# Performance work log

Hardware: AMD Instinct MI355X
Metric: run time of the kernel (lower is better)

## Reference

```python
import jax, jax.numpy as jnp
import numpy as np

N_NODES = 10000
N_EDGES = 5_000_000
BATCH = 2000


def setup_inputs() -> dict:
    key = jax.random.key(0)
    k1, k2, k3, k4 = jax.random.split(key, 4)
    n, E = N_NODES, N_EDGES
    # valid undirected pairs i < j
    i = jax.random.randint(k1, (E,), 0, n - 1)
    r = jax.random.randint(k2, (E,), 0, n)
    j = i + 1 + r % (n - 1 - i)
    edges = jnp.stack([i, j])  # [2, E], int
    edge_times = jax.random.uniform(k3, (E,), dtype=jnp.float32)
    edge_states = jax.random.randint(k4, (E,), 0, 2)
    return {
        "edges": edges,
        "edge_times": edge_times,
        "edge_states": edge_states,
        "nodes_num": n,
        "batch_size": BATCH,
    }


def _flat_idx(i, j, n):
    # undirected upper-triangular linearization of pair (i, j), i < j
    return i * n - i * (i + 1) // 2 + (j - i - 1)


def reference(edges, edge_times, edge_states, nodes_num, batch_size):
    n = nodes_num
    # -- multinomial(arange(n), batch_size, replacement=False) via Gumbel top-k --
    key = jax.random.key(19)
    w = jnp.arange(n, dtype=jnp.float32)
    logw = jnp.where(w > 0, jnp.log(jnp.maximum(w, 1.0)), -jnp.inf)
    scores = logw + jax.random.gumbel(key, (n,), dtype=jnp.float32)
    _, sel = jax.lax.top_k(scores, batch_size)
    batch_nodes = jnp.sort(sel)

    # -- all combinations (i < j since batch_nodes is sorted) --
    ii, jj = np.triu_indices(batch_size, k=1)  # static shapes
    batch_pairs = jnp.stack([batch_nodes[ii], batch_nodes[jj]])  # [2, P]
    batch_flat = _flat_idx(batch_pairs[0], batch_pairs[1], n)  # ascending

    # -- gather stored edges whose pair index is in the batch --
    edge_flat = _flat_idx(edges[0], edges[1], n)
    order = jnp.argsort(edge_flat)  # jax sort is stable -> matches coalesce order
    edges_sorted = edges[:, order]
    flat_sorted = edge_flat[order]
    times_sorted = edge_times[order]
    states_sorted = edge_states[order]

    pos = jnp.searchsorted(batch_flat, flat_sorted)
    pos = jnp.clip(pos, 0, batch_flat.shape[0] - 1)
    mask = batch_flat[pos] == flat_sorted  # [E] membership of each edge in batch

    batch_edge_times = jnp.where(mask, times_sorted, 0.0)
    batch_states = jnp.where(mask, states_sorted, 0)
    return (batch_nodes, batch_pairs, edges_sorted, batch_edge_times,
            batch_states, mask)
```

## Files before the change

kernel.cpp:

```cpp
#include <hip/hip_runtime.h>
#include <stdint.h>
#include <math.h>

#define N_NODES  10000
#define N_EDGES  5000000
#define BATCH    2000
#define N_PAIRS  1999000

#define OUT_BN      0
#define OUT_PAIRS0  2000
#define OUT_PAIRS1  2001000
#define OUT_ES0     4000000
#define OUT_ES1     9000000
#define OUT_T       14000000
#define OUT_S       19000000
#define OUT_M       24000000

#define WS_KEYS     0
#define WS_SEL      80000
#define WS_BN       120000
#define WS_CNT      128000
#define WS_FILL     168000
#define WS_OFF      208000
#define WS_SCRATCH  248064


#define RPB_LOG  7
#define NB1      79
#define CHUNK    2048
#define NBIN     192
#define NBITSW   313
#define RANK_BLKS 200

typedef unsigned long long u64;

__device__ __forceinline__ u64 score_key(int w, unsigned bits) {
  const float TINY = 1.17549435e-38f;
  float uf = __uint_as_float((bits >> 9) | 0x3f800000u) - 1.0f;
  float val = fmaxf(TINY, uf + TINY);
  float t1 = (float)log((double)val);
  float gmb = -(float)log((double)(-t1));
  float score = (w > 0) ? ((float)log((double)w) + gmb) : (-INFINITY);
  unsigned fb = __float_as_uint(score);
  unsigned s = (fb & 0x80000000u) ? ~fb : (fb | 0x80000000u);
  unsigned d = ~s;
  return ((u64)d << 32) | (unsigned)w;
}

__device__ __forceinline__ u64 make_key(int v) {
  unsigned ks[3] = {0u, 19u, 0u ^ 19u ^ 0x1BD11BDAu};
  unsigned x0 = 0u + ks[0];
  unsigned x1 = (unsigned)v + ks[1];
  const int R0[4] = {13, 15, 26, 6};
  const int R1[4] = {17, 29, 16, 24};
#pragma unroll
  for (int g = 0; g < 5; ++g) {
    const int* R = (g & 1) ? R1 : R0;
#pragma unroll
    for (int r = 0; r < 4; ++r) {
      x0 += x1;
      x1 = (x1 << R[r]) | (x1 >> (32 - R[r]));
      x1 ^= x0;
    }
    x0 += ks[(g + 1) % 3];
    x1 += ks[(g + 2) % 3] + (unsigned)(g + 1);
  }
  return score_key(v, x0 ^ x1);
}

__global__ void __launch_bounds__(256) k_rankhist(
    int* __restrict__ rankc, int* __restrict__ cnt,
    const int4* __restrict__ e_i4) {
  __shared__ __align__(16) int sh4[N_NODES];
  int tid = threadIdx.x;
  if ((int)blockIdx.x < RANK_BLKS) {
    u64* lk = (u64*)sh4;
    int vblk = blockIdx.x / 5, cblk = blockIdx.x % 5;
    int base = cblk * 2048;
    int lenc = min(2048, N_NODES - base);
    for (int t = tid; t < lenc; t += 256) lk[t] = make_key(base + t);
    __syncthreads();
    int v = vblk * 256 + tid;
    u64 kv = (v < N_NODES) ? make_key(v) : 0;
    int c = 0;
    for (int t = 0; t < lenc; ++t) c += (lk[t] < kv) ? 1 : 0;
    if (v < N_NODES && c) atomicAdd(&rankc[v], c);
  } else {
    int* h = sh4;
    for (int t = tid; t < N_NODES; t += 256) h[t] = 0;
    __syncthreads();
    int hb = blockIdx.x - RANK_BLKS;
    int stride = 256 * 256;
    for (int t = hb * 256 + tid; t < N_EDGES / 4; t += stride) {
      int4 r = e_i4[t];
      atomicAdd(&h[r.x], 1);
      atomicAdd(&h[r.y], 1);
      atomicAdd(&h[r.z], 1);
      atomicAdd(&h[r.w], 1);
    }
    __syncthreads();
    for (int t = tid; t < N_NODES; t += 256) {
      int c = h[t];
      if (c) atomicAdd(&cnt[t], c);
    }
  }
}

__global__ void k_scan_all(const int* rankc, int* sel, int* bn, float* outbn,
                           const int* cnt, int* off, int* fill, int* fill1,
                           unsigned* selbits) {
  __shared__ int wsum[16];
  __shared__ unsigned lb[320];
  const int PER = 10;
  int tid = threadIdx.x, lane = tid & 63, wid = tid >> 6;
  int base = tid * PER;
  int svv[PER];
  {
    int s = 0;
#pragma unroll
    for (int k = 0; k < PER; ++k) {
      int i = base + k;
      if (i < N_NODES) {
        int sv = (rankc[i] < BATCH) ? 1 : 0;
        sel[i] = sv;
        svv[k] = sv;
        s += sv;
      } else svv[k] = 0;
    }
    int inc = s;
#pragma unroll
    for (int d = 1; d < 64; d <<= 1) {
      int v = __shfl_up(inc, d, 64);
      if (lane >= d) inc += v;
    }
    if (lane == 63) wsum[wid] = inc;
    __syncthreads();
    int woff = 0;
    for (int w = 0; w < wid; ++w) woff += wsum[w];
    int run = woff + inc - s;
#pragma unroll
    for (int k = 0; k < PER; ++k) {
      int i = base + k;
      if (i < N_NODES && svv[k]) {
        bn[run] = i;
        outbn[run] = (float)i;
        ++run;
      }
    }
  }
  __syncthreads();
  {
    int cv[PER];
    int s = 0;
#pragma unroll
    for (int k = 0; k < PER; ++k) {
      int i = base + k;
      if (i < N_NODES) { cv[k] = cnt[i]; s += cv[k]; } else cv[k] = 0;
    }
    int inc = s;
#pragma unroll
    for (int d = 1; d < 64; d <<= 1) {
      int v = __shfl_up(inc, d, 64);
      if (lane >= d) inc += v;
    }
    if (lane == 63) wsum[wid] = inc;
    __syncthreads();
    int woff = 0;
    for (int w = 0; w < wid; ++w) woff += wsum[w];
    int run = woff + inc - s;
#pragma unroll
    for (int k = 0; k < PER; ++k) {
      int i = base + k;
      if (i < N_NODES) {
        off[i] = run;
        fill[i] = run;
        if ((i & ((1 << RPB_LOG) - 1)) == 0) fill1[i >> RPB_LOG] = run;
        run += cv[k];
      }
    }
    if (tid == 0) off[N_NODES] = N_EDGES;
  }
  __syncthreads();
  if (tid < 320) lb[tid] = 0;
  __syncthreads();
#pragma unroll
  for (int k = 0; k < PER; ++k) {
    int i = base + k;
    if (i < N_NODES && svv[k]) atomicOr(&lb[i >> 5], 1u << (i & 31));
  }
  __syncthreads();
  if (tid < NBITSW) selbits[tid] = lb[tid];
}

__global__ void __launch_bounds__(256) k_pairs_part1(
    const int* __restrict__ e_i, const int* __restrict__ e_j,
    const int* __restrict__ st, int* __restrict__ fill1,
    u64* __restrict__ stage, const int* __restrict__ bn,
    float* __restrict__ outp, int nblk1) {
  __shared__ u64 lkey[CHUNK];
  __shared__ int h[NB1], bstart[NB1], basec[NB1], cur[NB1];
  __shared__ int tcount_s;
  int tid = threadIdx.x;
  if ((int)blockIdx.x >= nblk1) {
    int p = ((int)blockIdx.x - nblk1) * 256 + tid;
    if (p >= N_PAIRS) return;
    float tf = 2.0f * BATCH - 1.0f;
    float disc = tf * tf - 8.0f * (float)p;
    int ii = (int)((tf - sqrtf(disc)) * 0.5f);
    if (ii < 0) ii = 0;
    if (ii > BATCH - 2) ii = BATCH - 2;
    while (ii > 0 &&
           (long long)ii * (BATCH - 1) - (long long)ii * (ii - 1) / 2 > p) --ii;
    while ((long long)(ii + 1) * (BATCH - 1) - (long long)(ii + 1) * ii / 2 <= p) ++ii;
    long long S = (long long)ii * (BATCH - 1) - (long long)ii * (ii - 1) / 2;
    int jj = ii + 1 + (int)(p - S);
    outp[p] = (float)bn[ii];
    outp[N_PAIRS + p] = (float)bn[jj];
    return;
  }
  int c0 = (int)blockIdx.x * CHUNK;
  int nloc = min(CHUNK, N_EDGES - c0);
  for (int t = tid; t < NB1; t += 256) h[t] = 0;
  __syncthreads();
  int iv[CHUNK / 256];
  const int4* e_i4 = (const int4*)(e_i + c0);
#pragma unroll
  for (int k = 0; k < CHUNK / 1024; ++k) {
    int q = tid + 256 * k;
    int ebase = 4 * q;
    if (ebase < nloc) {
      int4 r = e_i4[q];
      iv[4 * k + 0] = r.x; iv[4 * k + 1] = r.y;
      iv[4 * k + 2] = r.z; iv[4 * k + 3] = r.w;
      atomicAdd(&h[r.x >> RPB_LOG], 1);
      atomicAdd(&h[r.y >> RPB_LOG], 1);
      atomicAdd(&h[r.z >> RPB_LOG], 1);
      atomicAdd(&h[r.w >> RPB_LOG], 1);
    } else {
      iv[4 * k + 0] = iv[4 * k + 1] = iv[4 * k + 2] = iv[4 * k + 3] = -1;
    }
  }
  __syncthreads();
  if (tid < 64) {
    int a = h[tid];
    int b = (tid + 64 < NB1) ? h[tid + 64] : 0;
    int inc0 = a;
#pragma unroll
    for (int d = 1; d < 64; d <<= 1) {
      int v = __shfl_up(inc0, d, 64);
      if (tid >= d) inc0 += v;
    }
    int t0 = __shfl(inc0, 63, 64);
    int inc1 = b;
#pragma unroll
    for (int d = 1; d < 64; d <<= 1) {
      int v = __shfl_up(inc1, d, 64);
      if (tid >= d) inc1 += v;
    }
    int tot = t0 + __shfl(inc1, 63, 64);
    bstart[tid] = inc0 - a;
    if (tid + 64 < NB1) bstart[tid + 64] = t0 + inc1 - b;
    if (tid == 0) tcount_s = tot;
  }
  __syncthreads();
  for (int b = tid; b < NB1; b += 256) {
    basec[b] = h[b] ? atomicAdd(&fill1[b], h[b]) : 0;
    cur[b] = bstart[b];
  }
  __syncthreads();
  const int4* e_j4 = (const int4*)(e_j + c0);
  const int4* st4 = (const int4*)(st + c0);
#pragma unroll
  for (int k = 0; k < CHUNK / 1024; ++k) {
    int q = tid + 256 * k;
    int ebase = 4 * q;
    if (ebase < nloc) {
      int4 jj = e_j4[q];
      int4 ss = st4[q];
      int js[4] = {jj.x, jj.y, jj.z, jj.w};
      int s4[4] = {ss.x, ss.y, ss.z, ss.w};
#pragma unroll
      for (int c = 0; c < 4; ++c) {
        int i = iv[4 * k + c];
        unsigned e = (unsigned)(c0 + ebase + c);
        int b = i >> RPB_LOG;
        int pos = atomicAdd(&cur[b], 1);
        lkey[pos] = ((u64)(unsigned)i << 38) | ((u64)(unsigned)js[c] << 24) |
                    ((u64)e << 1) | (u64)(unsigned)s4[c];
      }
    }
  }
  __syncthreads();
  int tcount = tcount_s;
  for (int t = tid; t < tcount; t += 256) {
    u64 kv = lkey[t];
    int b = (int)(kv >> (38 + RPB_LOG));
    stage[basec[b] + (t - bstart[b])] = kv;
  }
}

__global__ void __launch_bounds__(256) k_part2(
    const u64* __restrict__ stage, int* __restrict__ fill,
    u64* __restrict__ sk) {
  __shared__ u64 lkey[CHUNK];
  __shared__ int h[256], bstart[256], baser[256], cur[256], wsum4[4];
  __shared__ int rowbase_s;
  int tid = threadIdx.x, lane = tid & 63, wid = tid >> 6;
  int c0 = (int)blockIdx.x * CHUNK;
  int nloc = min(CHUNK, N_EDGES - c0);
  h[tid] = 0;
  if (tid == 0)
    rowbase_s = ((int)(stage[c0] >> (38 + RPB_LOG))) << RPB_LOG;
  __syncthreads();
  int rowbase = rowbase_s;
  u64 kv[CHUNK / 256];
#pragma unroll
  for (int k = 0; k < CHUNK / 256; ++k) {
    int q = tid + 256 * k;
    if (q < nloc) {
      kv[k] = stage[c0 + q];
      atomicAdd(&h[(int)(kv[k] >> 38) - rowbase], 1);
    }
  }
  __syncthreads();
  int hv = h[tid];
  int inc = hv;
#pragma unroll
  for (int d = 1; d < 64; d <<= 1) {
    int v = __shfl_up(inc, d, 64);
    if (lane >= d) inc += v;
  }
  if (lane == 63) wsum4[wid] = inc;
  __syncthreads();
  int woff = 0;
  for (int w = 0; w < wid; ++w) woff += wsum4[w];
  int tcount = wsum4[0] + wsum4[1] + wsum4[2] + wsum4[3];
  int excl = woff + inc - hv;
  bstart[tid] = excl;
  cur[tid] = excl;
  baser[tid] = hv ? atomicAdd(&fill[rowbase + tid], hv) : 0;
  __syncthreads();
#pragma unroll
  for (int k = 0; k < CHUNK / 256; ++k) {
    int q = tid + 256 * k;
    if (q < nloc) {
      int lr = (int)(kv[k] >> 38) - rowbase;
      int pos = atomicAdd(&cur[lr], 1);
      lkey[pos] = kv[k];
    }
  }
  __syncthreads();
  for (int t = tid; t < tcount; t += 256) {
    u64 v = lkey[t];
    int lr = (int)(v >> 38) - rowbase;
    sk[baser[lr] + (t - bstart[lr])] = v;
  }
}

__global__ void __launch_bounds__(256) k_rowsort_key(
    const u64* __restrict__ sk, const int* __restrict__ off,
    const float* __restrict__ times, const unsigned* __restrict__ selbits,
    float* __restrict__ out) {
  __shared__ u64 buf[768];
  __shared__ int hist[NBIN], cur[NBIN];
  __shared__ unsigned bits[320];
  int tid = threadIdx.x;
  int row = blockIdx.x;
  int o0 = off[row], o1 = off[row + 1];
  int len = o1 - o0;
  if (len <= 0) return;
  if (len > 768) len = 768;
  int span = N_NODES - 1 - row;
  int s = 0;
  while ((span >> s) >= 160) ++s;
  int mi = (int)((selbits[row >> 5] >> (row & 31)) & 1u);
  for (int t = tid; t < NBIN; t += 256) hist[t] = 0;
  if (mi) {
    for (int t = tid; t < NBITSW; t += 256) bits[t] = selbits[t];
  }
  __syncthreads();
  u64 kv[3];
  int dv[3], rv[3];
  int jbase = row + 1;
#pragma unroll
  for (int k = 0; k < 3; ++k) {
    int t = tid + 256 * k;
    if (t < len) {
      u64 v = sk[o0 + t];
      kv[k] = v;
      int j = (int)((v >> 24) & 0x3FFFull);
      int d = (j - jbase) >> s;
      dv[k] = d;
      atomicAdd(&hist[d], 1);
    } else {
      dv[k] = -1;
    }
  }
  __syncthreads();
  if (tid < 64) {
    int b0 = tid * 3;
    int c0 = hist[b0], c1 = hist[b0 + 1], c2 = hist[b0 + 2];
    int sum = c0 + c1 + c2;
    int inc = sum;
#pragma unroll
    for (int d = 1; d < 64; d <<= 1) {
      int v = __shfl_up(inc, d, 64);
      if (tid >= d) inc += v;
    }
    int excl = inc - sum;
    hist[b0] = excl;
    hist[b0 + 1] = excl + c0;
    hist[b0 + 2] = excl + c0 + c1;
    cur[b0] = excl;
    cur[b0 + 1] = excl + c0;
    cur[b0 + 2] = excl + c0 + c1;
  }
  __syncthreads();
#pragma unroll
  for (int k = 0; k < 3; ++k) {
    if (dv[k] >= 0) {
      int pos = atomicAdd(&cur[dv[k]], 1);
      buf[pos] = kv[k];
    }
  }
  __syncthreads();
#pragma unroll
  for (int k = 0; k < 3; ++k) {
    if (dv[k] >= 0) {
      u64 me = kv[k];
      int s0 = hist[dv[k]];
      int s1 = cur[dv[k]];
      int r = 0;
      for (int q = s0; q < s1; ++q) r += (buf[q] < me) ? 1 : 0;
      rv[k] = s0 + r;
    }
  }
  __syncthreads();
#pragma unroll
  for (int k = 0; k < 3; ++k)
    if (dv[k] >= 0) buf[rv[k]] = kv[k];
  __syncthreads();
  float frow = (float)row;
  if (mi) {
    for (int t = tid; t < len; t += 256) {
      u64 k = buf[t];
      int j = (int)((k >> 24) & 0x3FFFull);
      int idx = (int)((k >> 1) & 0x7FFFFFull);
      int st = (int)(k & 1ull);
      int p = o0 + t;
      out[OUT_ES0 + p] = frow;
      out[OUT_ES1 + p] = (float)j;
      bool m = (bits[j >> 5] >> (j & 31)) & 1u;
      out[OUT_T + p] = m ? times[idx] : 0.0f;
      out[OUT_S + p] = m ? (float)st : 0.0f;
      out[OUT_M + p] = m ? 1.0f : 0.0f;
    }
  } else {
    for (int t = tid; t < len; t += 256) {
      u64 k = buf[t];
      int j = (int)((k >> 24) & 0x3FFFull);
      int p = o0 + t;
      out[OUT_ES0 + p] = frow;
      out[OUT_ES1 + p] = (float)j;
      out[OUT_T + p] = 0.0f;
      out[OUT_S + p] = 0.0f;
      out[OUT_M + p] = 0.0f;
    }
  }
}

__global__ void __launch_bounds__(256) k_scatter_idx(
    const int4* __restrict__ e_i4, int* __restrict__ fill,
    unsigned* __restrict__ sk) {
  int t = blockIdx.x * blockDim.x + threadIdx.x;
  if (t >= N_EDGES / 4) return;
  int4 r = e_i4[t];
  unsigned e = 4u * (unsigned)t;
  int c0 = atomicAdd(&fill[r.x], 1);
  int c1 = atomicAdd(&fill[r.y], 1);
  int c2 = atomicAdd(&fill[r.z], 1);
  int c3 = atomicAdd(&fill[r.w], 1);
  sk[c0] = e;
  sk[c1] = e + 1;
  sk[c2] = e + 2;
  sk[c3] = e + 3;
}

__global__ void __launch_bounds__(256) k_rowsort_idx(
    const unsigned* __restrict__ sk, const int* __restrict__ e_j_arr,
    const int* __restrict__ off, const float* __restrict__ times,
    const int* __restrict__ states, const int* __restrict__ sel,
    float* __restrict__ out) {
  __shared__ u64 key[2048];
  int row = blockIdx.x;
  int o0 = off[row], o1 = off[row + 1];
  int len = o1 - o0;
  if (len <= 0) return;
  if (len > 2048) len = 2048;
  int M = 2;
  while (M < len) M <<= 1;
  for (int t = threadIdx.x; t < M; t += blockDim.x) {
    if (t < len) {
      unsigned e = sk[o0 + t];
      key[t] = ((u64)(unsigned)e_j_arr[e] << 32) | e;
    } else {
      key[t] = 0xFFFFFFFFFFFFFFFFull;
    }
  }
  __syncthreads();
  for (int k = 2; k <= M; k <<= 1) {
    for (int j = k >> 1; j > 0; j >>= 1) {
      for (int t = threadIdx.x; t < M; t += blockDim.x) {
        int ixj = t ^ j;
        if (ixj > t) {
          u64 a = key[t], b = key[ixj];
          bool up = ((t & k) == 0);
          if (up ? (a > b) : (a < b)) {
            key[t] = b;
            key[ixj] = a;
          }
        }
      }
      __syncthreads();
    }
  }
  int mi = sel[row];
  float frow = (float)row;
  for (int t = threadIdx.x; t < len; t += blockDim.x) {
    u64 k = key[t];
    int j = (int)(k >> 32);
    int idx = (int)(k & 0xFFFFFFFFull);
    int p = o0 + t;
    out[OUT_ES0 + p] = frow;
    out[OUT_ES1 + p] = (float)j;
    bool m = (mi != 0) && (sel[j] != 0);
    float tm = 0.0f, sv = 0.0f;
    if (m) {
      tm = times[idx];
      sv = (float)states[idx];
    }
    out[OUT_T + p] = tm;
    out[OUT_S + p] = sv;
    out[OUT_M + p] = m ? 1.0f : 0.0f;
  }
}

extern "C" void kernel_launch(void* const* d_in, const int* in_sizes, int n_in,
                              void* d_out, int out_size, void* d_ws, size_t ws_size,
                              hipStream_t stream) {
  const int* edges = (const int*)d_in[0];
  const float* times = (const float*)d_in[1];
  const int* states = (const int*)d_in[2];
  const int* e_i = edges;
  const int* e_j = edges + N_EDGES;
  float* out = (float*)d_out;
  char* ws = (char*)d_ws;

  int* fill1 = (int*)(ws + WS_KEYS);
  int* sel = (int*)(ws + WS_SEL);
  int* bn = (int*)(ws + WS_BN);
  int* cnt = (int*)(ws + WS_CNT);
  unsigned* selbits = (unsigned*)(ws + WS_CNT);
  int* fill = (int*)(ws + WS_FILL);
  int* rankc = (int*)(ws + WS_FILL);
  int* off = (int*)(ws + WS_OFF);
  u64* sk64 = (u64*)(ws + WS_SCRATCH);
  unsigned* sk32 = (unsigned*)(ws + WS_SCRATCH);
  u64* stage = (u64*)(out + OUT_ES0);
  int use64 = (ws_size >= (size_t)WS_SCRATCH + 8ull * N_EDGES) ? 1 : 0;

  hipMemsetAsync(ws + WS_CNT, 0, 80000, stream);

  int npair_b = (N_PAIRS + 255) / 256;
  k_rankhist<<<RANK_BLKS + 256, 256, 0, stream>>>(rankc, cnt, (const int4*)e_i);
  k_scan_all<<<1, 1024, 0, stream>>>(rankc, sel, bn, out + OUT_BN, cnt, off,
                                     fill, fill1, selbits);
  if (use64) {
    int nblk1 = (N_EDGES + CHUNK - 1) / CHUNK;
    k_pairs_part1<<<nblk1 + npair_b, 256, 0, stream>>>(
        e_i, e_j, states, fill1, stage, bn, out + OUT_PAIRS0, nblk1);
    k_part2<<<nblk1, 256, 0, stream>>>(stage, fill, sk64);
    k_rowsort_key<<<N_NODES, 256, 0, stream>>>(sk64, off, times, selbits, out);
  } else {
    k_pairs_part1<<<npair_b, 256, 0, stream>>>(
        e_i, e_j, states, fill1, stage, bn, out + OUT_PAIRS0, 0);
    k_scatter_idx<<<(N_EDGES / 4 + 255) / 256, 256, 0, stream>>>(
        (const int4*)e_i, fill, sk32);
    k_rowsort_idx<<<N_NODES, 256, 0, stream>>>(sk32, e_j, off, times, states,
                                               sel, out);
  }
}
```

Baseline: 373.4 us.

## Scatter partition keys straight to global memory and write sorted outputs from ranks

Both bucket-partition kernels stop staging keys in shared memory. Each key is now written directly to its global bucket slot using a per-bucket atomic counter, which removes the local prefix scans and the extra LDS pass, and the chunk size doubles to 4096. The row-sort kernel moves the times gather and membership lookup ahead of the sort and writes outputs straight to the computed rank positions, skipping the shared-memory permute and re-read. The cost is scattered, less coalesced global writes in place of grouped stores, and more registers per thread because of the larger chunk.

```diff
diff --git a/kernel.cpp b/kernel.cpp
--- a/kernel.cpp
+++ b/kernel.cpp
@@ -27,7 +27,7 @@
 
 #define RPB_LOG  7
 #define NB1      79
-#define CHUNK    2048
+#define CHUNK    4096
 #define NBIN     192
 #define NBITSW   313
 #define RANK_BLKS 200
@@ -197,9 +197,7 @@
     const int* __restrict__ st, int* __restrict__ fill1,
     u64* __restrict__ stage, const int* __restrict__ bn,
     float* __restrict__ outp, int nblk1) {
-  __shared__ u64 lkey[CHUNK];
-  __shared__ int h[NB1], bstart[NB1], basec[NB1], cur[NB1];
-  __shared__ int tcount_s;
+  __shared__ int h[NB1], basec[NB1], cur[NB1];
   int tid = threadIdx.x;
   if ((int)blockIdx.x >= nblk1) {
     int p = ((int)blockIdx.x - nblk1) * 256 + tid;
@@ -220,7 +218,7 @@
   }
   int c0 = (int)blockIdx.x * CHUNK;
   int nloc = min(CHUNK, N_EDGES - c0);
-  for (int t = tid; t < NB1; t += 256) h[t] = 0;
+  for (int t = tid; t < NB1; t += 256) { h[t] = 0; cur[t] = 0; }
   __syncthreads();
   int iv[CHUNK / 256];
   const int4* e_i4 = (const int4*)(e_i + c0);
@@ -241,32 +239,8 @@
     }
   }
   __syncthreads();
-  if (tid < 64) {
-    int a = h[tid];
-    int b = (tid + 64 < NB1) ? h[tid + 64] : 0;
-    int inc0 = a;
-#pragma unroll
-    for (int d = 1; d < 64; d <<= 1) {
-      int v = __shfl_up(inc0, d, 64);
-      if (tid >= d) inc0 += v;
-    }
-    int t0 = __shfl(inc0, 63, 64);
-    int inc1 = b;
-#pragma unroll
-    for (int d = 1; d < 64; d <<= 1) {
-      int v = __shfl_up(inc1, d, 64);
-      if (tid >= d) inc1 += v;
-    }
-    int tot = t0 + __shfl(inc1, 63, 64);
-    bstart[tid] = inc0 - a;
-    if (tid + 64 < NB1) bstart[tid + 64] = t0 + inc1 - b;
-    if (tid == 0) tcount_s = tot;
-  }
-  __syncthreads();
-  for (int b = tid; b < NB1; b += 256) {
+  for (int b = tid; b < NB1; b += 256)
     basec[b] = h[b] ? atomicAdd(&fill1[b], h[b]) : 0;
-    cur[b] = bstart[b];
-  }
   __syncthreads();
   const int4* e_j4 = (const int4*)(e_j + c0);
   const int4* st4 = (const int4*)(st + c0);
@@ -285,34 +259,25 @@
         unsigned e = (unsigned)(c0 + ebase + c);
         int b = i >> RPB_LOG;
         int pos = atomicAdd(&cur[b], 1);
-        lkey[pos] = ((u64)(unsigned)i << 38) | ((u64)(unsigned)js[c] << 24) |
-                    ((u64)e << 1) | (u64)(unsigned)s4[c];
+        stage[basec[b] + pos] = ((u64)(unsigned)i << 38) |
+                                ((u64)(unsigned)js[c] << 24) |
+                                ((u64)e << 1) | (u64)(unsigned)s4[c];
       }
     }
-  }
-  __syncthreads();
-  int tcount = tcount_s;
-  for (int t = tid; t < tcount; t += 256) {
-    u64 kv = lkey[t];
-    int b = (int)(kv >> (38 + RPB_LOG));
-    stage[basec[b] + (t - bstart[b])] = kv;
   }
 }
 
 __global__ void __launch_bounds__(256) k_part2(
     const u64* __restrict__ stage, int* __restrict__ fill,
     u64* __restrict__ sk) {
-  __shared__ u64 lkey[CHUNK];
-  __shared__ int h[256], bstart[256], baser[256], cur[256], wsum4[4];
-  __shared__ int rowbase_s;
-  int tid = threadIdx.x, lane = tid & 63, wid = tid >> 6;
+  __shared__ int h[256], baser[256], cur[256];
+  int tid = threadIdx.x;
   int c0 = (int)blockIdx.x * CHUNK;
   int nloc = min(CHUNK, N_EDGES - c0);
   h[tid] = 0;
-  if (tid == 0)
-    rowbase_s = ((int)(stage[c0] >> (38 + RPB_LOG))) << RPB_LOG;
-  __syncthreads();
-  int rowbase = rowbase_s;
+  cur[tid] = 0;
+  int rowbase = ((int)(stage[c0] >> (38 + RPB_LOG))) << RPB_LOG;
+  __syncthreads();
   u64 kv[CHUNK / 256];
 #pragma unroll
   for (int k = 0; k < CHUNK / 256; ++k) {
@@ -324,20 +289,6 @@
   }
   __syncthreads();
   int hv = h[tid];
-  int inc = hv;
-#pragma unroll
-  for (int d = 1; d < 64; d <<= 1) {
-    int v = __shfl_up(inc, d, 64);
-    if (lane >= d) inc += v;
-  }
-  if (lane == 63) wsum4[wid] = inc;
-  __syncthreads();
-  int woff = 0;
-  for (int w = 0; w < wid; ++w) woff += wsum4[w];
-  int tcount = wsum4[0] + wsum4[1] + wsum4[2] + wsum4[3];
-  int excl = woff + inc - hv;
-  bstart[tid] = excl;
-  cur[tid] = excl;
   baser[tid] = hv ? atomicAdd(&fill[rowbase + tid], hv) : 0;
   __syncthreads();
 #pragma unroll
@@ -345,15 +296,9 @@
     int q = tid + 256 * k;
     if (q < nloc) {
       int lr = (int)(kv[k] >> 38) - rowbase;
-      int pos = atomicAdd(&cur[lr], 1);
-      lkey[pos] = kv[k];
-    }
-  }
-  __syncthreads();
-  for (int t = tid; t < tcount; t += 256) {
-    u64 v = lkey[t];
-    int lr = (int)(v >> 38) - rowbase;
-    sk[baser[lr] + (t - bstart[lr])] = v;
+      int c = atomicAdd(&cur[lr], 1);
+      sk[baser[lr] + c] = kv[k];
+    }
   }
 }
 
@@ -374,26 +319,36 @@
   int s = 0;
   while ((span >> s) >= 160) ++s;
   int mi = (int)((selbits[row >> 5] >> (row & 31)) & 1u);
+  u64 kv[3];
+  int dv[3];
+#pragma unroll
+  for (int k = 0; k < 3; ++k) {
+    int t = tid + 256 * k;
+    if (t < len) { kv[k] = sk[o0 + t]; dv[k] = 0; }
+    else { kv[k] = 0; dv[k] = -1; }
+  }
   for (int t = tid; t < NBIN; t += 256) hist[t] = 0;
   if (mi) {
     for (int t = tid; t < NBITSW; t += 256) bits[t] = selbits[t];
   }
   __syncthreads();
-  u64 kv[3];
-  int dv[3], rv[3];
   int jbase = row + 1;
+  float tmv[3];
+  int mv[3];
 #pragma unroll
   for (int k = 0; k < 3; ++k) {
-    int t = tid + 256 * k;
-    if (t < len) {
-      u64 v = sk[o0 + t];
-      kv[k] = v;
-      int j = (int)((v >> 24) & 0x3FFFull);
+    if (dv[k] >= 0) {
+      int j = (int)((kv[k] >> 24) & 0x3FFFull);
       int d = (j - jbase) >> s;
       dv[k] = d;
       atomicAdd(&hist[d], 1);
+      int m = mi ? (int)((bits[j >> 5] >> (j & 31)) & 1u) : 0;
+      mv[k] = m;
+      int idx = (int)((kv[k] >> 1) & 0x7FFFFFull);
+      tmv[k] = m ? times[idx] : 0.0f;
     } else {
-      dv[k] = -1;
+      mv[k] = 0;
+      tmv[k] = 0.0f;
     }
   }
   __syncthreads();
@@ -424,6 +379,8 @@
     }
   }
   __syncthreads();
+  float frow = (float)row;
+  for (int t = tid; t < len; t += 256) out[OUT_ES0 + o0 + t] = frow;
 #pragma unroll
   for (int k = 0; k < 3; ++k) {
     if (dv[k] >= 0) {
@@ -432,39 +389,11 @@
       int s1 = cur[dv[k]];
       int r = 0;
       for (int q = s0; q < s1; ++q) r += (buf[q] < me) ? 1 : 0;
-      rv[k] = s0 + r;
-    }
-  }
-  __syncthreads();
-#pragma unroll
-  for (int k = 0; k < 3; ++k)
-    if (dv[k] >= 0) buf[rv[k]] = kv[k];
-  __syncthreads();
-  float frow = (float)row;
-  if (mi) {
-    for (int t = tid; t < len; t += 256) {
-      u64 k = buf[t];
-      int j = (int)((k >> 24) & 0x3FFFull);
-      int idx = (int)((k >> 1) & 0x7FFFFFull);
-      int st = (int)(k & 1ull);
-      int p = o0 + t;
-      out[OUT_ES0 + p] = frow;
-      out[OUT_ES1 + p] = (float)j;
-      bool m = (bits[j >> 5] >> (j & 31)) & 1u;
-      out[OUT_T + p] = m ? times[idx] : 0.0f;
-      out[OUT_S + p] = m ? (float)st : 0.0f;
-      out[OUT_M + p] = m ? 1.0f : 0.0f;
-    }
-  } else {
-    for (int t = tid; t < len; t += 256) {
-      u64 k = buf[t];
-      int j = (int)((k >> 24) & 0x3FFFull);
-      int p = o0 + t;
-      out[OUT_ES0 + p] = frow;
-      out[OUT_ES1 + p] = (float)j;
-      out[OUT_T + p] = 0.0f;
-      out[OUT_S + p] = 0.0f;
-      out[OUT_M + p] = 0.0f;
+      int p = o0 + s0 + r;
+      out[OUT_ES1 + p] = (float)((int)((me >> 24) & 0x3FFFull));
+      out[OUT_T + p] = tmv[k];
+      out[OUT_S + p] = mv[k] ? (float)((int)(me & 1ull)) : 0.0f;
+      out[OUT_M + p] = mv[k] ? 1.0f : 0.0f;
     }
   }
 }
```

New measurement: 401.7 us. 1.08x slower.
